# Kernel tuning notes

Measured on AMD Instinct MI355X. Metric: run time of the kernel, lower is better.

The kernel has to match this reference:

```python
import jax, jax.numpy as jnp
import numpy as np

B, T, D = 256, 512, 128


def setup_inputs() -> dict:
    key = jax.random.key(0)
    ks = jax.random.split(key, 10)
    s = 0.05
    return {
        "x": jax.random.normal(ks[0], (B, T, D), jnp.float32),
        "lengths": jax.random.randint(ks[1], (B,), 1, T + 1, dtype=jnp.int32),
        "Wa": jax.random.normal(ks[2], (D, 3 * D), jnp.float32) * s,
        "Ua": jax.random.normal(ks[3], (D, 3 * D), jnp.float32) * s,
        "ba_in": jnp.zeros((3 * D,), jnp.float32),
        "ba_rec": jnp.zeros((3 * D,), jnp.float32),
        "Wb": jax.random.normal(ks[4], (D, 3 * D), jnp.float32) * s,
        "Ub": jax.random.normal(ks[5], (D, 3 * D), jnp.float32) * s,
        "bb_in": jnp.zeros((3 * D,), jnp.float32),
        "bb_rec": jnp.zeros((3 * D,), jnp.float32),
        "W_alpha": jax.random.normal(ks[6], (D, 1), jnp.float32) * s,
        "b_alpha": jnp.zeros((1,), jnp.float32),
        "W_beta": jax.random.normal(ks[7], (D, D), jnp.float32) * s,
        "b_beta": jnp.zeros((D,), jnp.float32),
    }


def _masked_gru(xp, mask_t, U, b_rec):
    # Keras GRU v2 (reset_after=True). xp: [T,B,3D] input projections (+input bias),
    # mask_t: [T,B]. Masked steps carry state forward (Keras mask semantics).
    h0 = jnp.zeros((xp.shape[1], U.shape[0]), xp.dtype)

    def step(h, inp):
        xt, mt = inp
        rp = h @ U + b_rec                      # [B,3D] recurrent projection
        xz, xr, xh = jnp.split(xt, 3, axis=-1)
        rz, rr, rh = jnp.split(rp, 3, axis=-1)
        z = jax.nn.sigmoid(xz + rz)
        r = jax.nn.sigmoid(xr + rr)
        hh = jnp.tanh(xh + r * rh)
        hn = z * h + (1.0 - z) * hh
        hn = jnp.where(mt[:, None], hn, h)
        return hn, hn

    _, hs = jax.lax.scan(step, h0, (xp, mask_t))
    return hs  # [T,B,D]


def _forward(x, lengths, Wa, Ua, ba_in, ba_rec, Wb, Ub, bb_in, bb_rec,
             W_alpha, b_alpha, W_beta, b_beta):
    Tn = x.shape[1]
    t = jnp.arange(Tn)
    valid = t[None, :] < lengths[:, None]                      # [B,T]
    # vectorized per-sample reverse of the first `length` steps, zeros after
    ridx = jnp.clip(lengths[:, None] - 1 - t[None, :], 0, Tn - 1)
    rx = jnp.take_along_axis(x, ridx[:, :, None], axis=1)
    rx = jnp.where(valid[:, :, None], rx, jnp.zeros((), x.dtype))

    mask_t = valid.T                                            # [T,B]
    g = _masked_gru(jnp.einsum('btd,de->tbe', rx, Wa) + ba_in, mask_t, Ua, ba_rec)
    h = _masked_gru(jnp.einsum('btd,de->tbe', rx, Wb) + bb_in, mask_t, Ub, bb_rec)
    g = jnp.transpose(g, (1, 0, 2))                             # [B,T,D]
    h = jnp.transpose(h, (1, 0, 2))

    attn_alpha = jax.nn.softmax(g @ W_alpha + b_alpha, axis=1)  # [B,T,1] over time
    attn_beta = jnp.tanh(h @ W_beta + b_beta)                   # [B,T,D]
    return jnp.sum(attn_alpha * attn_beta * x, axis=1)          # [B,D]


def reference(x, lengths, Wa, Ua, ba_in, ba_rec, Wb, Ub, bb_in, bb_rec,
              W_alpha, b_alpha, W_beta, b_beta):
    return _forward(x, lengths, Wa, Ua, ba_in, ba_rec, Wb, Ub, bb_in, bb_rec,
                    W_alpha, b_alpha, W_beta, b_beta)
```

## Files before the change

kernel.cpp:

```cpp
#include <hip/hip_runtime.h>
#include <hip/hip_fp16.h>
#include <math.h>


#define BATCH 256
#define TLEN  512
#define DDIM  128
#define G3    384

static const size_t HB_SZ = (size_t)BATCH * TLEN * DDIM;
static const size_t E_SZ  = (size_t)BATCH * TLEN;

__device__ __forceinline__ int clamp_len(int l) {
    return l < 1 ? 1 : (l > TLEN ? TLEN : l);
}
__device__ __forceinline__ float sigm_f(float s) {
    s = fminf(fmaxf(s, -30.f), 30.f);
    return __fdividef(1.f, 1.f + __expf(-s));
}
__device__ __forceinline__ float tanh_f(float u) {
    u = fminf(fmaxf(u, -15.f), 15.f);
    const float e2 = __expf(2.f * u);
    return __fdividef(e2 - 1.f, e2 + 1.f);
}

__global__ __launch_bounds__(768, 3) void retain_gru_v3(
    const float* __restrict__ x, const int* __restrict__ lengths,
    const float* __restrict__ Wa, const float* __restrict__ Ua,
    const float* __restrict__ ba_in, const float* __restrict__ ba_rec,
    const float* __restrict__ Wb, const float* __restrict__ Ub,
    const float* __restrict__ bb_in, const float* __restrict__ bb_rec,
    const float* __restrict__ W_alpha, const float* __restrict__ b_alpha,
    __half* __restrict__ hB, float* __restrict__ e)
{
    const int g   = blockIdx.x & 1;
    const int ip  = blockIdx.x >> 1;
    const int tid = threadIdx.x;
    const int m   = (tid >= 384) ? 1 : 0;
    const int tp  = tid - 384 * m;
    const int q   = tp / 96;
    const int c4  = (tp - q * 96) * 4;

    __shared__ int lensh[BATCH];
    __shared__ int rank2b[BATCH];
    __shared__ __align__(16) float xsh[2][DDIM];
    __shared__ __align__(16) float hsh[2][DDIM];
    __shared__ __align__(16) float parts[2][4][G3];
    __shared__ __align__(16) float walsh[DDIM];
    __shared__ __align__(16) float ep8[2][8];

    if (tid < BATCH) lensh[tid] = clamp_len(lengths[tid]);
    if (tid < DDIM)  walsh[tid] = W_alpha[tid];
    __syncthreads();
    if (tid < BATCH) {
        const int myl = lensh[tid];
        int rank = 0;
        for (int j = 0; j < BATCH; ++j) {
            const int lj = lensh[j];
            rank += (lj > myl) || (lj == myl && j < tid);
        }
        rank2b[rank] = tid;
    }

    const float* __restrict__ Mw = m ? (g ? Ub : Ua) : (g ? Wb : Wa);
    float W0[32], W1[32], W2[32], W3[32];
    #pragma unroll
    for (int r = 0; r < 32; ++r) {
        const float4 wv = *reinterpret_cast<const float4*>(Mw + (size_t)(q * 32 + r) * G3 + c4);
        W0[r] = wv.x; W1[r] = wv.y; W2[r] = wv.z; W3[r] = wv.w;
    }

    float bi0 = 0, bi1 = 0, bi2 = 0, br0 = 0, br1 = 0, br2 = 0, balv = 0;
    if (tid < DDIM) {
        const float* bi = g ? bb_in  : ba_in;
        const float* br = g ? bb_rec : ba_rec;
        bi0 = bi[tid]; bi1 = bi[tid + 128]; bi2 = bi[tid + 256];
        br0 = br[tid]; br1 = br[tid + 128]; br2 = br[tid + 256];
    }
    if (tid == 136) balv = b_alpha[0];
    __syncthreads();

    for (int jj = 0; jj < 2; ++jj) {
        const int b   = rank2b[jj ? 255 - ip : ip];
        const int len = lensh[b];
        if (tid < DDIM) {
            hsh[1][tid] = 0.f;
            xsh[0][tid] = x[((size_t)b * TLEN + (len - 1)) * DDIM + tid];
        }
        __syncthreads();

        for (int t = 0; t < len; ++t) {
            float xnext = 0.f;
            if (tid < DDIM) {
                int rn = len - 2 - t; if (rn < 0) rn = 0;
                xnext = x[((size_t)b * TLEN + rn) * DDIM + tid];
            }
            const float* __restrict__ vh = (m ? hsh[(t + 1) & 1] : xsh[t & 1]) + q * 32;
            float A0 = 0.f, A1 = 0.f, A2 = 0.f, A3 = 0.f;
            #pragma unroll
            for (int rr = 0; rr < 32; rr += 4) {
                const float4 v = *reinterpret_cast<const float4*>(vh + rr);
                A0 = fmaf(v.x, W0[rr+0], A0); A1 = fmaf(v.x, W1[rr+0], A1);
                A2 = fmaf(v.x, W2[rr+0], A2); A3 = fmaf(v.x, W3[rr+0], A3);
                A0 = fmaf(v.y, W0[rr+1], A0); A1 = fmaf(v.y, W1[rr+1], A1);
                A2 = fmaf(v.y, W2[rr+1], A2); A3 = fmaf(v.y, W3[rr+1], A3);
                A0 = fmaf(v.z, W0[rr+2], A0); A1 = fmaf(v.z, W1[rr+2], A1);
                A2 = fmaf(v.z, W2[rr+2], A2); A3 = fmaf(v.z, W3[rr+2], A3);
                A0 = fmaf(v.w, W0[rr+3], A0); A1 = fmaf(v.w, W1[rr+3], A1);
                A2 = fmaf(v.w, W2[rr+3], A2); A3 = fmaf(v.w, W3[rr+3], A3);
            }
            *reinterpret_cast<float4*>(&parts[m][q][c4]) = float4{A0, A1, A2, A3};
            __syncthreads();

            if (tid < DDIM) {
                const int d = tid;
                const float xz = bi0 + parts[0][0][d]     + parts[0][1][d]     + parts[0][2][d]     + parts[0][3][d];
                const float xr = bi1 + parts[0][0][128+d] + parts[0][1][128+d] + parts[0][2][128+d] + parts[0][3][128+d];
                const float xh = bi2 + parts[0][0][256+d] + parts[0][1][256+d] + parts[0][2][256+d] + parts[0][3][256+d];
                const float rz = br0 + parts[1][0][d]     + parts[1][1][d]     + parts[1][2][d]     + parts[1][3][d];
                const float rr_= br1 + parts[1][0][128+d] + parts[1][1][128+d] + parts[1][2][128+d] + parts[1][3][128+d];
                const float rh = br2 + parts[1][0][256+d] + parts[1][1][256+d] + parts[1][2][256+d] + parts[1][3][256+d];
                const float z  = sigm_f(xz + rz);
                const float r_ = sigm_f(xr + rr_);
                const float hh = tanh_f(xh + r_ * rh);
                const float hn = z * hsh[(t + 1) & 1][d] + (1.f - z) * hh;
                hsh[t & 1][d] = hn;
                xsh[(t + 1) & 1][d] = xnext;
                if (g) hB[((size_t)b * TLEN + t) * DDIM + d] = __float2half(hn);
            } else if (!g && tid >= 128 && tid < 136) {
                if (t >= 1) {
                    const int k0 = (tid - 128) * 16;
                    const float* hp = hsh[(t + 1) & 1];
                    float s = 0.f;
                    #pragma unroll
                    for (int i2 = 0; i2 < 16; i2 += 4) {
                        const float4 hv = *reinterpret_cast<const float4*>(hp + k0 + i2);
                        const float4 wv = *reinterpret_cast<const float4*>(&walsh[k0 + i2]);
                        s = fmaf(hv.w, wv.w, fmaf(hv.z, wv.z, fmaf(hv.y, wv.y, fmaf(hv.x, wv.x, s))));
                    }
                    ep8[(t + 1) & 1][tid - 128] = s;
                }
            } else if (!g && tid == 136 && t >= 2) {
                float s = balv;
                #pragma unroll
                for (int i2 = 0; i2 < 8; ++i2) s += ep8[t & 1][i2];
                e[(size_t)b * TLEN + (t - 2)] = s;
            }
            asm volatile("s_waitcnt lgkmcnt(0)" ::: "memory");
            __builtin_amdgcn_s_barrier();
            __builtin_amdgcn_sched_barrier(0);
        }

        if (!g && tid >= 128 && tid < 136) {
            const int k0 = (tid - 128) * 16;
            const float* hp = hsh[(len + 1) & 1];
            float s = 0.f;
            #pragma unroll
            for (int i2 = 0; i2 < 16; i2 += 4) {
                const float4 hv = *reinterpret_cast<const float4*>(hp + k0 + i2);
                const float4 wv = *reinterpret_cast<const float4*>(&walsh[k0 + i2]);
                s = fmaf(hv.w, wv.w, fmaf(hv.z, wv.z, fmaf(hv.y, wv.y, fmaf(hv.x, wv.x, s))));
            }
            ep8[(len + 1) & 1][tid - 128] = s;
        } else if (!g && tid == 136 && len >= 2) {
            float s = balv;
            #pragma unroll
            for (int i2 = 0; i2 < 8; ++i2) s += ep8[len & 1][i2];
            e[(size_t)b * TLEN + (len - 2)] = s;
        }
        __syncthreads();
        if (!g && tid == 136) {
            float s = balv;
            #pragma unroll
            for (int i2 = 0; i2 < 8; ++i2) s += ep8[(len + 1) & 1][i2];
            e[(size_t)b * TLEN + (len - 1)] = s;
        }
        __syncthreads();
    }
}

__global__ __launch_bounds__(256, 4) void retain_attn_h(
    const float* __restrict__ x, const int* __restrict__ lengths,
    const float* __restrict__ W_beta, const float* __restrict__ b_beta,
    const __half* __restrict__ hB, const float* __restrict__ eb,
    float* __restrict__ out)
{
    const int bid = blockIdx.x;
    const int b   = bid >> 2;
    const int tq  = bid & 3;
    const int len = clamp_len(lengths[b]);
    const float* __restrict__ e = eb + (size_t)b * TLEN;

    const int tid = threadIdx.x;
    const int d   = tid & 127;
    const int rh  = tid >> 7;

    float Wreg[64];
    #pragma unroll
    for (int rr = 0; rr < 64; rr++) Wreg[rr] = W_beta[(rh * 64 + rr) * DDIM + d];
    const float bb = b_beta[d];

    __shared__ float se[512];
    __shared__ float red[256];
    __shared__ __align__(16) float h2[2][128];
    __shared__ float part[2][2][128];

    for (int idx = tid; idx < 512; idx += 256) {
        const int tc = idx < len ? idx : len - 1;
        se[idx] = e[tc];
    }
    __syncthreads();
    red[tid] = fmaxf(se[tid], se[tid + 256]);
    __syncthreads();
    for (int s = 128; s > 0; s >>= 1) {
        if (tid < s) red[tid] = fmaxf(red[tid], red[tid + s]);
        __syncthreads();
    }
    const float mx = red[0];
    __syncthreads();
    const float s0 = expf(se[tid] - mx), s1 = expf(se[tid + 256] - mx);
    se[tid] = s0; se[tid + 256] = s1;
    red[tid] = s0 + s1;
    __syncthreads();
    for (int s = 128; s > 0; s >>= 1) {
        if (tid < s) red[tid] += red[tid + s];
        __syncthreads();
    }
    const float inv = 1.f / red[0];
    __syncthreads();

    const int tbase = tq * 128;
    float acc = 0.f;
    for (int tp = 0; tp < 128; tp += 2) {
        const int t0 = tbase + tp;
        {
            const int t  = t0 + rh;
            const int tc = t < len ? t : len - 1;
            h2[rh][d] = __half2float(hB[((size_t)b * TLEN + tc) * DDIM + d]);
        }
        __syncthreads();
        float p0 = 0.f, p1 = 0.f;
        #pragma unroll
        for (int rr = 0; rr < 64; rr += 4) {
            const float4 ha = *reinterpret_cast<const float4*>(&h2[0][rh * 64 + rr]);
            const float4 hb = *reinterpret_cast<const float4*>(&h2[1][rh * 64 + rr]);
            p0 = fmaf(ha.x, Wreg[rr + 0], p0);
            p0 = fmaf(ha.y, Wreg[rr + 1], p0);
            p0 = fmaf(ha.z, Wreg[rr + 2], p0);
            p0 = fmaf(ha.w, Wreg[rr + 3], p0);
            p1 = fmaf(hb.x, Wreg[rr + 0], p1);
            p1 = fmaf(hb.y, Wreg[rr + 1], p1);
            p1 = fmaf(hb.z, Wreg[rr + 2], p1);
            p1 = fmaf(hb.w, Wreg[rr + 3], p1);
        }
        part[rh][0][d] = p0;
        part[rh][1][d] = p1;
        __syncthreads();
        if (rh == 0) {
            #pragma unroll
            for (int ti = 0; ti < 2; ti++) {
                const int t = t0 + ti;
                const float v  = tanhf(part[0][ti][d] + part[1][ti][d] + bb);
                const float al = se[t] * inv;
                const float xv = x[((size_t)b * TLEN + t) * DDIM + d];
                acc = fmaf(al * v, xv, acc);
            }
        }
        __syncthreads();
    }
    if (rh == 0) atomicAdd(&out[b * DDIM + d], acc);
}

extern "C" void kernel_launch(void* const* d_in, const int* in_sizes, int n_in,
                              void* d_out, int out_size, void* d_ws, size_t ws_size,
                              hipStream_t stream)
{
    const float* x       = (const float*)d_in[0];
    const int*   lengths = (const int*)  d_in[1];
    const float* Wa      = (const float*)d_in[2];
    const float* Ua      = (const float*)d_in[3];
    const float* ba_in   = (const float*)d_in[4];
    const float* ba_rec  = (const float*)d_in[5];
    const float* Wb      = (const float*)d_in[6];
    const float* Ub      = (const float*)d_in[7];
    const float* bb_in   = (const float*)d_in[8];
    const float* bb_rec  = (const float*)d_in[9];
    const float* W_alpha = (const float*)d_in[10];
    const float* b_alpha = (const float*)d_in[11];
    const float* W_beta  = (const float*)d_in[12];
    const float* b_beta  = (const float*)d_in[13];
    float* out = (float*)d_out;

    const size_t need = HB_SZ * sizeof(__half) + E_SZ * sizeof(float);
    if (ws_size < need) return;

    __half* hB = (__half*)d_ws;
    float*  e  = (float*)((char*)d_ws + HB_SZ * sizeof(__half));

    hipMemsetAsync(d_out, 0, (size_t)out_size * sizeof(float), stream);
    retain_gru_v3<<<256, 768, 0, stream>>>(
        x, lengths, Wa, Ua, ba_in, ba_rec, Wb, Ub, bb_in, bb_rec, W_alpha, b_alpha, hB, e);
    retain_attn_h<<<1024, 256, 0, stream>>>(x, lengths, W_beta, b_beta, hB, e, out);
}
```

Baseline: 1.090 ms.

## Use fp16 packed dot2 GRU matvec with one sequence per block

```diff
diff --git a/kernel.cpp b/kernel.cpp
--- a/kernel.cpp
+++ b/kernel.cpp
@@ -8,6 +8,14 @@
 #define DDIM  128
 #define G3    384
 
+typedef _Float16 half2_t __attribute__((ext_vector_type(2)));
+
+#if defined(__has_builtin) && __has_builtin(__builtin_amdgcn_fdot2)
+#define FDOT2(a, b, c) __builtin_amdgcn_fdot2((a), (b), (c), false)
+#else
+#define FDOT2(a, b, c) fmaf((float)(a)[0], (float)(b)[0], fmaf((float)(a)[1], (float)(b)[1], (c)))
+#endif
+
 static const size_t HB_SZ = (size_t)BATCH * TLEN * DDIM;
 static const size_t E_SZ  = (size_t)BATCH * TLEN;
 
@@ -24,7 +32,7 @@
     return __fdividef(e2 - 1.f, e2 + 1.f);
 }
 
-__global__ __launch_bounds__(768, 3) void retain_gru_v3(
+__global__ __launch_bounds__(512, 4) void retain_gru_h2(
     const float* __restrict__ x, const int* __restrict__ lengths,
     const float* __restrict__ Wa, const float* __restrict__ Ua,
     const float* __restrict__ ba_in, const float* __restrict__ ba_rec,
@@ -33,24 +41,33 @@
     const float* __restrict__ W_alpha, const float* __restrict__ b_alpha,
     __half* __restrict__ hB, float* __restrict__ e)
 {
-    const int g   = blockIdx.x & 1;
-    const int ip  = blockIdx.x >> 1;
+    const int bid = blockIdx.x;
+    const int g   = bid >> 8;
+    const int rk  = bid & 255;
     const int tid = threadIdx.x;
-    const int m   = (tid >= 384) ? 1 : 0;
-    const int tp  = tid - 384 * m;
-    const int q   = tp / 96;
-    const int c4  = (tp - q * 96) * 4;
+    const int m   = (tid >= 256) ? 1 : 0;
+    const int tt  = tid & 255;
+    const int half= tt >> 7;
+    const int c   = tt & 127;
 
     __shared__ int lensh[BATCH];
     __shared__ int rank2b[BATCH];
-    __shared__ __align__(16) float xsh[2][DDIM];
-    __shared__ __align__(16) float hsh[2][DDIM];
-    __shared__ __align__(16) float parts[2][4][G3];
+    __shared__ __align__(16) _Float16 xsh16[DDIM];
+    __shared__ __align__(16) _Float16 hsh16[DDIM];
+    __shared__ __align__(16) float hsh32[2][DDIM];
+    __shared__ __align__(16) float parts[2][2][G3];
     __shared__ __align__(16) float walsh[DDIM];
+    __shared__ __align__(16) float bxsh[G3];
+    __shared__ __align__(16) float bush[G3];
     __shared__ __align__(16) float ep8[2][8];
 
     if (tid < BATCH) lensh[tid] = clamp_len(lengths[tid]);
     if (tid < DDIM)  walsh[tid] = W_alpha[tid];
+    {
+        const float* bi = g ? bb_in  : ba_in;
+        const float* br = g ? bb_rec : ba_rec;
+        for (int i = tid; i < G3; i += 512) { bxsh[i] = bi[i]; bush[i] = br[i]; }
+    }
     __syncthreads();
     if (tid < BATCH) {
         const int myl = lensh[tid];
@@ -61,121 +78,120 @@
         }
         rank2b[rank] = tid;
     }
+    float balv = 0.f;
+    if (tid == 136) balv = b_alpha[0];
+    __syncthreads();
+
+    const int b   = rank2b[rk];
+    const int len = lensh[b];
 
     const float* __restrict__ Mw = m ? (g ? Ub : Ua) : (g ? Wb : Wa);
-    float W0[32], W1[32], W2[32], W3[32];
+    half2_t W0[32], W1[32], W2[32];
     #pragma unroll
-    for (int r = 0; r < 32; ++r) {
-        const float4 wv = *reinterpret_cast<const float4*>(Mw + (size_t)(q * 32 + r) * G3 + c4);
-        W0[r] = wv.x; W1[r] = wv.y; W2[r] = wv.z; W3[r] = wv.w;
-    }
-
-    float bi0 = 0, bi1 = 0, bi2 = 0, br0 = 0, br1 = 0, br2 = 0, balv = 0;
+    for (int j = 0; j < 32; ++j) {
+        const float* r0 = Mw + (size_t)(half * 64 + 2 * j) * G3 + c;
+        const float* r1 = r0 + G3;
+        W0[j] = (half2_t){(_Float16)r0[0],   (_Float16)r1[0]};
+        W1[j] = (half2_t){(_Float16)r0[128], (_Float16)r1[128]};
+        W2[j] = (half2_t){(_Float16)r0[256], (_Float16)r1[256]};
+    }
+
     if (tid < DDIM) {
-        const float* bi = g ? bb_in  : ba_in;
-        const float* br = g ? bb_rec : ba_rec;
-        bi0 = bi[tid]; bi1 = bi[tid + 128]; bi2 = bi[tid + 256];
-        br0 = br[tid]; br1 = br[tid + 128]; br2 = br[tid + 256];
-    }
-    if (tid == 136) balv = b_alpha[0];
-    __syncthreads();
-
-    for (int jj = 0; jj < 2; ++jj) {
-        const int b   = rank2b[jj ? 255 - ip : ip];
-        const int len = lensh[b];
+        hsh32[1][tid] = 0.f;
+        hsh16[tid]    = (_Float16)0.f;
+        xsh16[tid]    = (_Float16)x[((size_t)b * TLEN + (len - 1)) * DDIM + tid];
+    }
+    __syncthreads();
+
+    for (int t = 0; t < len; ++t) {
+        float xnext = 0.f;
         if (tid < DDIM) {
-            hsh[1][tid] = 0.f;
-            xsh[0][tid] = x[((size_t)b * TLEN + (len - 1)) * DDIM + tid];
-        }
-        __syncthreads();
-
-        for (int t = 0; t < len; ++t) {
-            float xnext = 0.f;
-            if (tid < DDIM) {
-                int rn = len - 2 - t; if (rn < 0) rn = 0;
-                xnext = x[((size_t)b * TLEN + rn) * DDIM + tid];
+            int rn = len - 2 - t; if (rn < 0) rn = 0;
+            xnext = x[((size_t)b * TLEN + rn) * DDIM + tid];
+        }
+        const uint* __restrict__ vhu =
+            reinterpret_cast<const uint*>(m ? hsh16 : xsh16) + half * 32;
+        float A0 = 0.f, A1 = 0.f, A2 = 0.f;
+        #pragma unroll
+        for (int j = 0; j < 32; j += 4) {
+            const uint4 v = *reinterpret_cast<const uint4*>(vhu + j);
+            const half2_t p0 = __builtin_bit_cast(half2_t, v.x);
+            const half2_t p1 = __builtin_bit_cast(half2_t, v.y);
+            const half2_t p2 = __builtin_bit_cast(half2_t, v.z);
+            const half2_t p3 = __builtin_bit_cast(half2_t, v.w);
+            A0 = FDOT2(p0, W0[j+0], A0); A1 = FDOT2(p0, W1[j+0], A1); A2 = FDOT2(p0, W2[j+0], A2);
+            A0 = FDOT2(p1, W0[j+1], A0); A1 = FDOT2(p1, W1[j+1], A1); A2 = FDOT2(p1, W2[j+1], A2);
+            A0 = FDOT2(p2, W0[j+2], A0); A1 = FDOT2(p2, W1[j+2], A1); A2 = FDOT2(p2, W2[j+2], A2);
+            A0 = FDOT2(p3, W0[j+3], A0); A1 = FDOT2(p3, W1[j+3], A1); A2 = FDOT2(p3, W2[j+3], A2);
+        }
+        parts[m][half][c]       = A0;
+        parts[m][half][c + 128] = A1;
+        parts[m][half][c + 256] = A2;
+        __syncthreads();
+
+        if (tid < DDIM) {
+            const int d = tid;
+            const float xz = bxsh[d]       + parts[0][0][d]       + parts[0][1][d];
+            const float xr = bxsh[128 + d] + parts[0][0][128 + d] + parts[0][1][128 + d];
+            const float xh = bxsh[256 + d] + parts[0][0][256 + d] + parts[0][1][256 + d];
+            const float rz = bush[d]       + parts[1][0][d]       + parts[1][1][d];
+            const float rr_= bush[128 + d] + parts[1][0][128 + d] + parts[1][1][128 + d];
+            const float rh = bush[256 + d] + parts[1][0][256 + d] + parts[1][1][256 + d];
+            const float z  = sigm_f(xz + rz);
+            const float r_ = sigm_f(xr + rr_);
+            const float hh = tanh_f(xh + r_ * rh);
+            const float hn = z * hsh32[(t + 1) & 1][d] + (1.f - z) * hh;
+            hsh32[t & 1][d] = hn;
+            hsh16[d] = (_Float16)hn;
+            xsh16[d] = (_Float16)xnext;
+            if (g) hB[((size_t)b * TLEN + t) * DDIM + d] = __float2half(hn);
+        } else if (!g && tid >= 128 && tid < 136) {
+            if (t >= 1) {
+                const int k0 = (tid - 128) * 16;
+                const float* hp = hsh32[(t + 1) & 1];
+                float s = 0.f;
+                #pragma unroll
+                for (int i2 = 0; i2 < 16; i2 += 4) {
+                    const float4 hv = *reinterpret_cast<const float4*>(hp + k0 + i2);
+                    const float4 wv = *reinterpret_cast<const float4*>(&walsh[k0 + i2]);
+                    s = fmaf(hv.w, wv.w, fmaf(hv.z, wv.z, fmaf(hv.y, wv.y, fmaf(hv.x, wv.x, s))));
+                }
+                ep8[(t + 1) & 1][tid - 128] = s;
             }
-            const float* __restrict__ vh = (m ? hsh[(t + 1) & 1] : xsh[t & 1]) + q * 32;
-            float A0 = 0.f, A1 = 0.f, A2 = 0.f, A3 = 0.f;
-            #pragma unroll
-            for (int rr = 0; rr < 32; rr += 4) {
-                const float4 v = *reinterpret_cast<const float4*>(vh + rr);
-                A0 = fmaf(v.x, W0[rr+0], A0); A1 = fmaf(v.x, W1[rr+0], A1);
-                A2 = fmaf(v.x, W2[rr+0], A2); A3 = fmaf(v.x, W3[rr+0], A3);
-                A0 = fmaf(v.y, W0[rr+1], A0); A1 = fmaf(v.y, W1[rr+1], A1);
-                A2 = fmaf(v.y, W2[rr+1], A2); A3 = fmaf(v.y, W3[rr+1], A3);
-                A0 = fmaf(v.z, W0[rr+2], A0); A1 = fmaf(v.z, W1[rr+2], A1);
-                A2 = fmaf(v.z, W2[rr+2], A2); A3 = fmaf(v.z, W3[rr+2], A3);
-                A0 = fmaf(v.w, W0[rr+3], A0); A1 = fmaf(v.w, W1[rr+3], A1);
-                A2 = fmaf(v.w, W2[rr+3], A2); A3 = fmaf(v.w, W3[rr+3], A3);
-            }
-            *reinterpret_cast<float4*>(&parts[m][q][c4]) = float4{A0, A1, A2, A3};
-            __syncthreads();
-
-            if (tid < DDIM) {
-                const int d = tid;
-                const float xz = bi0 + parts[0][0][d]     + parts[0][1][d]     + parts[0][2][d]     + parts[0][3][d];
-                const float xr = bi1 + parts[0][0][128+d] + parts[0][1][128+d] + parts[0][2][128+d] + parts[0][3][128+d];
-                const float xh = bi2 + parts[0][0][256+d] + parts[0][1][256+d] + parts[0][2][256+d] + parts[0][3][256+d];
-                const float rz = br0 + parts[1][0][d]     + parts[1][1][d]     + parts[1][2][d]     + parts[1][3][d];
-                const float rr_= br1 + parts[1][0][128+d] + parts[1][1][128+d] + parts[1][2][128+d] + parts[1][3][128+d];
-                const float rh = br2 + parts[1][0][256+d] + parts[1][1][256+d] + parts[1][2][256+d] + parts[1][3][256+d];
-                const float z  = sigm_f(xz + rz);
-                const float r_ = sigm_f(xr + rr_);
-                const float hh = tanh_f(xh + r_ * rh);
-                const float hn = z * hsh[(t + 1) & 1][d] + (1.f - z) * hh;
-                hsh[t & 1][d] = hn;
-                xsh[(t + 1) & 1][d] = xnext;
-                if (g) hB[((size_t)b * TLEN + t) * DDIM + d] = __float2half(hn);
-            } else if (!g && tid >= 128 && tid < 136) {
-                if (t >= 1) {
-                    const int k0 = (tid - 128) * 16;
-                    const float* hp = hsh[(t + 1) & 1];
-                    float s = 0.f;
-                    #pragma unroll
-                    for (int i2 = 0; i2 < 16; i2 += 4) {
-                        const float4 hv = *reinterpret_cast<const float4*>(hp + k0 + i2);
-                        const float4 wv = *reinterpret_cast<const float4*>(&walsh[k0 + i2]);
-                        s = fmaf(hv.w, wv.w, fmaf(hv.z, wv.z, fmaf(hv.y, wv.y, fmaf(hv.x, wv.x, s))));
-                    }
-                    ep8[(t + 1) & 1][tid - 128] = s;
-                }
-            } else if (!g && tid == 136 && t >= 2) {
-                float s = balv;
-                #pragma unroll
-                for (int i2 = 0; i2 < 8; ++i2) s += ep8[t & 1][i2];
-                e[(size_t)b * TLEN + (t - 2)] = s;
-            }
-            asm volatile("s_waitcnt lgkmcnt(0)" ::: "memory");
-            __builtin_amdgcn_s_barrier();
-            __builtin_amdgcn_sched_barrier(0);
-        }
-
-        if (!g && tid >= 128 && tid < 136) {
-            const int k0 = (tid - 128) * 16;
-            const float* hp = hsh[(len + 1) & 1];
-            float s = 0.f;
-            #pragma unroll
-            for (int i2 = 0; i2 < 16; i2 += 4) {
-                const float4 hv = *reinterpret_cast<const float4*>(hp + k0 + i2);
-                const float4 wv = *reinterpret_cast<const float4*>(&walsh[k0 + i2]);
-                s = fmaf(hv.w, wv.w, fmaf(hv.z, wv.z, fmaf(hv.y, wv.y, fmaf(hv.x, wv.x, s))));
-            }
-            ep8[(len + 1) & 1][tid - 128] = s;
-        } else if (!g && tid == 136 && len >= 2) {
+        } else if (!g && tid == 136 && t >= 2) {
             float s = balv;
             #pragma unroll
-            for (int i2 = 0; i2 < 8; ++i2) s += ep8[len & 1][i2];
-            e[(size_t)b * TLEN + (len - 2)] = s;
-        }
-        __syncthreads();
-        if (!g && tid == 136) {
-            float s = balv;
-            #pragma unroll
-            for (int i2 = 0; i2 < 8; ++i2) s += ep8[(len + 1) & 1][i2];
-            e[(size_t)b * TLEN + (len - 1)] = s;
-        }
-        __syncthreads();
+            for (int i2 = 0; i2 < 8; ++i2) s += ep8[t & 1][i2];
+            e[(size_t)b * TLEN + (t - 2)] = s;
+        }
+        asm volatile("s_waitcnt lgkmcnt(0)" ::: "memory");
+        __builtin_amdgcn_s_barrier();
+        __builtin_amdgcn_sched_barrier(0);
+    }
+
+    if (!g && tid >= 128 && tid < 136) {
+        const int k0 = (tid - 128) * 16;
+        const float* hp = hsh32[(len + 1) & 1];
+        float s = 0.f;
+        #pragma unroll
+        for (int i2 = 0; i2 < 16; i2 += 4) {
+            const float4 hv = *reinterpret_cast<const float4*>(hp + k0 + i2);
+            const float4 wv = *reinterpret_cast<const float4*>(&walsh[k0 + i2]);
+            s = fmaf(hv.w, wv.w, fmaf(hv.z, wv.z, fmaf(hv.y, wv.y, fmaf(hv.x, wv.x, s))));
+        }
+        ep8[(len + 1) & 1][tid - 128] = s;
+    } else if (!g && tid == 136 && len >= 2) {
+        float s = balv;
+        #pragma unroll
+        for (int i2 = 0; i2 < 8; ++i2) s += ep8[len & 1][i2];
+        e[(size_t)b * TLEN + (len - 2)] = s;
+    }
+    __syncthreads();
+    if (!g && tid == 136) {
+        float s = balv;
+        #pragma unroll
+        for (int i2 = 0; i2 < 8; ++i2) s += ep8[(len + 1) & 1][i2];
+        e[(size_t)b * TLEN + (len - 1)] = s;
     }
 }
 
@@ -298,7 +314,7 @@
     float*  e  = (float*)((char*)d_ws + HB_SZ * sizeof(__half));
 
     hipMemsetAsync(d_out, 0, (size_t)out_size * sizeof(float), stream);
-    retain_gru_v3<<<256, 768, 0, stream>>>(
+    retain_gru_h2<<<512, 512, 0, stream>>>(
         x, lengths, Wa, Ua, ba_in, ba_rec, Wb, Ub, bb_in, bb_rec, W_alpha, b_alpha, hB, e);
     retain_attn_h<<<1024, 256, 0, stream>>>(x, lengths, W_beta, b_beta, hB, e, out);
 }
```

Result: slower. 1.168 ms (+7.2%).
